# Kernel optimization log

Measured on AMD Instinct MI355X. Metric: run time of the kernel, lower is better.

## Reference

```python
import jax, jax.numpy as jnp
import numpy as np

N = 50000      # nodes
E = 800000     # edges
D_IN = 128
D_H = 128
D_OUT = 64
P = 0.3        # dropout prob


def _glorot(key, out_c, in_c):
    return jax.random.normal(key, (out_c, in_c), jnp.float32) * (1.0 / np.sqrt(in_c))


def setup_inputs() -> dict:
    key = jax.random.key(0)
    ks = jax.random.split(key, 10)
    return {
        "x": jax.random.normal(ks[0], (N, D_IN), jnp.float32),
        "u1": jax.random.uniform(ks[1], (N, D_H), jnp.float32),
        "u2": jax.random.uniform(ks[2], (N, D_H), jnp.float32),
        "wl0": _glorot(ks[3], D_H, D_IN), "bl0": jnp.zeros((D_H,), jnp.float32), "wr0": _glorot(ks[4], D_H, D_IN),
        "wl1": _glorot(ks[5], D_H, D_H), "bl1": jnp.zeros((D_H,), jnp.float32), "wr1": _glorot(ks[6], D_H, D_H),
        "wl2": _glorot(ks[7], D_OUT, D_H), "bl2": jnp.zeros((D_OUT,), jnp.float32), "wr2": _glorot(ks[8], D_OUT, D_H),
        "edge_index": jax.random.randint(ks[9], (2, E), 0, N),
    }


def _sage_conv(x, src, dst, wl, bl, wr):
    # PyG SAGEConv (aggr='mean'): lin_l(mean of neighbor msgs) + lin_r(x)
    msg = x[src]                                                    # [E, d] gather
    s = jax.ops.segment_sum(msg, dst, num_segments=N)               # [N, d] scatter-sum
    cnt = jax.ops.segment_sum(jnp.ones((dst.shape[0],), x.dtype), dst, num_segments=N)
    mean = s / jnp.maximum(cnt, 1.0)[:, None]                       # mean; 0 for isolated nodes
    return mean @ wl.T + bl + x @ wr.T


def reference(x, u1, u2, wl0, bl0, wr0, wl1, bl1, wr1, wl2, bl2, wr2, edge_index):
    src, dst = edge_index[0], edge_index[1]
    keep = 1.0 - P
    h = jax.nn.relu(_sage_conv(x, src, dst, wl0, bl0, wr0))
    h = h * ((u1 >= P).astype(h.dtype) / keep)                      # dropout (training=True)
    h = jax.nn.relu(_sage_conv(h, src, dst, wl1, bl1, wr1))
    h = h * ((u2 >= P).astype(h.dtype) / keep)
    return _sage_conv(h, src, dst, wl2, bl2, wr2)
```

## Files before the change

kernel.cpp:

```cpp
#include <hip/hip_runtime.h>


constexpr int N = 50000;
constexpr int E = 800000;
constexpr int NBUCK = (N + 255) / 256;
constexpr int CE = 4096;
constexpr int NEB = (E + CE - 1) / CE;
constexpr int SLOT = 5120;
static_assert(N <= 65536, "u16 packing");

typedef _Float16 f16x8 __attribute__((ext_vector_type(8)));
typedef _Float16 f16x2 __attribute__((ext_vector_type(2)));
typedef float f32x4 __attribute__((ext_vector_type(4)));


__global__ __launch_bounds__(256) void bucket_scatter_kernel(
    const int* __restrict__ src, const int* __restrict__ dst,
    int* __restrict__ bcur, unsigned* __restrict__ T) {
  __shared__ unsigned sorted[CE];
  __shared__ int hist[256], scan[256], excl[256], lcur[256], gbase[256];
  const int t = threadIdx.x;
  const int e0 = blockIdx.x * CE;
  const int nval = min(CE, E - e0);
  hist[t] = 0;
  __syncthreads();
  for (int i = t; i < nval; i += 256) atomicAdd(&hist[dst[e0 + i] >> 8], 1);
  __syncthreads();
  const int h = hist[t];
  scan[t] = h;
  __syncthreads();
  for (int off = 1; off < 256; off <<= 1) {
    int u = (t >= off) ? scan[t - off] : 0;
    __syncthreads();
    scan[t] += u;
    __syncthreads();
  }
  excl[t] = scan[t] - h;
  lcur[t] = scan[t] - h;
  gbase[t] = (t < NBUCK && h > 0) ? atomicAdd(&bcur[t], h) : 0;
  __syncthreads();
  for (int i = t; i < nval; i += 256) {
    int e = e0 + i;
    int d = dst[e];
    int p = atomicAdd(&lcur[d >> 8], 1);
    sorted[p] = ((unsigned)d << 16) | (unsigned)src[e];
  }
  __syncthreads();
  for (int i = t; i < nval; i += 256) {
    unsigned pk = sorted[i];
    int b = pk >> 24;
    T[gbase[b] + (i - excl[b])] = pk;
  }
}

__global__ __launch_bounds__(256) void bucket_place_kernel(
    const unsigned* __restrict__ T, const int* __restrict__ bcur,
    int* __restrict__ offs, int* __restrict__ deg, int* __restrict__ elist) {
  __shared__ int dcnt[256], s[256], ncur[256];
  const int t = threadIdx.x;
  const int b = blockIdx.x;
  const int lo = b * SLOT;
  const int hi = bcur[b];
  dcnt[t] = 0;
  __syncthreads();
  for (int i = lo + t; i < hi; i += 256) atomicAdd(&dcnt[(T[i] >> 16) & 255], 1);
  __syncthreads();
  const int v = dcnt[t];
  s[t] = v;
  __syncthreads();
  for (int off = 1; off < 256; off <<= 1) {
    int u = (t >= off) ? s[t - off] : 0;
    __syncthreads();
    s[t] += u;
    __syncthreads();
  }
  const int base = lo + s[t] - v;
  const int node = b * 256 + t;
  if (node < N) { offs[node] = base; deg[node] = v; }
  ncur[t] = base;
  __syncthreads();
  for (int i = lo + t; i < hi; i += 256) {
    unsigned pk = T[i];
    int pos = atomicAdd(&ncur[(pk >> 16) & 255], 1);
    elist[pos] = (int)(pk & 0xffffu);
  }
}

__device__ inline void wfrag_build(int idx, int KB, const float* wl,
                                   const float* wr, _Float16* wf) {
  int j = idx & 7;
  int lane = (idx >> 3) & 63;
  int kb = (idx >> 9) % KB;
  int ct = (idx >> 9) / KB;
  int c = ct * 16 + (lane & 15);
  int k = kb * 32 + (lane >> 4) * 8 + j;
  float v = (k < 128) ? wl[c * 128 + k] : wr[c * 128 + (k - 128)];
  wf[idx] = (_Float16)v;
}

constexpr int CONVB = (N * 128 / 8 + 255) / 256;

__global__ __launch_bounds__(256) void setup_kernel(
    const float* __restrict__ x,
    const float* __restrict__ wl0, const float* __restrict__ wr0,
    const float* __restrict__ wl1, const float* __restrict__ wr1,
    const float* __restrict__ wl2, const float* __restrict__ wr2,
    _Float16* __restrict__ HA, _Float16* __restrict__ wf0,
    _Float16* __restrict__ wf1, _Float16* __restrict__ wfZ,
    int* __restrict__ bcur) {
  const int b = blockIdx.x;
  const int t = threadIdx.x;
  if (b < CONVB) {
    int i = b * 256 + t;
    if (i < N * 128 / 8) {
      float4 a = ((const float4*)x)[i * 2];
      float4 c = ((const float4*)x)[i * 2 + 1];
      f16x8 v;
      v[0] = (_Float16)a.x; v[1] = (_Float16)a.y; v[2] = (_Float16)a.z; v[3] = (_Float16)a.w;
      v[4] = (_Float16)c.x; v[5] = (_Float16)c.y; v[6] = (_Float16)c.z; v[7] = (_Float16)c.w;
      ((f16x8*)HA)[i] = v;
    }
  } else if (b < CONVB + 128) {
    wfrag_build((b - CONVB) * 256 + t, 8, wl0, wr0, wf0);
  } else if (b < CONVB + 256) {
    wfrag_build((b - CONVB - 128) * 256 + t, 8, wl1, wr1, wf1);
  } else if (b < CONVB + 320) {
    int idx = (b - CONVB - 256) * 256 + t;
    int j = idx & 7;
    int lane = (idx >> 3) & 63;
    int kb = (idx >> 9) & 3;
    int ct = idx >> 11;
    int c = ct * 16 + (lane & 15);
    int k = kb * 32 + (lane >> 4) * 8 + j;
    float v = (c < 64) ? wl2[c * 128 + k] : wr2[(c - 64) * 128 + k];
    wfZ[idx] = (_Float16)v;
  } else {
    if (t < NBUCK) bcur[t] = t * SLOT;
  }
}

__global__ __launch_bounds__(256) void gather128_kernel(
    const _Float16* __restrict__ H, const int* __restrict__ offs,
    const int* __restrict__ deg, const int* __restrict__ elist,
    _Float16* __restrict__ M) {
  int node = blockIdx.x * 4 + (threadIdx.x >> 6);
  if (node >= N) return;
  int l = threadIdx.x & 63;
  const int e0 = offs[node];
  const int d = deg[node];
  const int e1 = e0 + d;
  float a0 = 0.f, a1 = 0.f;
  int e = e0;
  for (; e + 16 <= e1; e += 16) {
    int s[16];
#pragma unroll
    for (int u = 0; u < 16; ++u) s[u] = elist[e + u];
    f16x2 v[16];
#pragma unroll
    for (int u = 0; u < 16; ++u)
      v[u] = *(const f16x2*)(H + (size_t)s[u] * 128 + l * 2);
#pragma unroll
    for (int u = 0; u < 16; ++u) { a0 += (float)v[u][0]; a1 += (float)v[u][1]; }
  }
  for (; e + 4 <= e1; e += 4) {
    int s[4];
#pragma unroll
    for (int u = 0; u < 4; ++u) s[u] = elist[e + u];
    f16x2 v[4];
#pragma unroll
    for (int u = 0; u < 4; ++u)
      v[u] = *(const f16x2*)(H + (size_t)s[u] * 128 + l * 2);
#pragma unroll
    for (int u = 0; u < 4; ++u) { a0 += (float)v[u][0]; a1 += (float)v[u][1]; }
  }
  for (; e < e1; ++e) {
    f16x2 v = *(const f16x2*)(H + (size_t)elist[e] * 128 + l * 2);
    a0 += (float)v[0]; a1 += (float)v[1];
  }
  float inv = 1.0f / (float)max(d, 1);
  f16x2 o;
  o[0] = (_Float16)(a0 * inv); o[1] = (_Float16)(a1 * inv);
  *(f16x2*)(M + (size_t)node * 128 + l * 2) = o;
}

__global__ __launch_bounds__(256) void gather64_add_kernel(
    const _Float16* __restrict__ Y2, const float* __restrict__ F,
    const int* __restrict__ offs, const int* __restrict__ deg,
    const int* __restrict__ elist, float* __restrict__ out) {
  int node = blockIdx.x * 8 + (threadIdx.x >> 5);
  if (node >= N) return;
  int l = threadIdx.x & 31;
  const int e0 = offs[node];
  const int d = deg[node];
  const int e1 = e0 + d;
  float a0 = 0.f, a1 = 0.f;
  int e = e0;
  for (; e + 16 <= e1; e += 16) {
    int s[16];
#pragma unroll
    for (int u = 0; u < 16; ++u) s[u] = elist[e + u];
    f16x2 v[16];
#pragma unroll
    for (int u = 0; u < 16; ++u)
      v[u] = *(const f16x2*)(Y2 + (size_t)s[u] * 64 + l * 2);
#pragma unroll
    for (int u = 0; u < 16; ++u) { a0 += (float)v[u][0]; a1 += (float)v[u][1]; }
  }
  for (; e + 4 <= e1; e += 4) {
    int s[4];
#pragma unroll
    for (int u = 0; u < 4; ++u) s[u] = elist[e + u];
    f16x2 v[4];
#pragma unroll
    for (int u = 0; u < 4; ++u)
      v[u] = *(const f16x2*)(Y2 + (size_t)s[u] * 64 + l * 2);
#pragma unroll
    for (int u = 0; u < 4; ++u) { a0 += (float)v[u][0]; a1 += (float)v[u][1]; }
  }
  for (; e < e1; ++e) {
    f16x2 v = *(const f16x2*)(Y2 + (size_t)elist[e] * 64 + l * 2);
    a0 += (float)v[0]; a1 += (float)v[1];
  }
  float inv = 1.0f / (float)max(d, 1);
  float2 f = ((const float2*)(F + (size_t)node * 64))[l];
  float2 o;
  o.x = f.x + a0 * inv;
  o.y = f.y + a1 * inv;
  ((float2*)(out + (size_t)node * 64))[l] = o;
}

__global__ __launch_bounds__(256, 4) void mfma_gemm128_kernel(
    const _Float16* __restrict__ Mm, const _Float16* __restrict__ Hh,
    const _Float16* __restrict__ Wf, const float* __restrict__ bias,
    const float* __restrict__ U, _Float16* __restrict__ outp) {
  const int lane = threadIdx.x & 63;
  const int w = threadIdx.x >> 6;
  const int n16 = lane & 15;
  const int q = lane >> 4;
  const int rowbase = blockIdx.x * 32;
  const int colbase = w * 32;

  f32x4 acc[2][2];
#pragma unroll
  for (int h = 0; h < 2; ++h)
#pragma unroll
    for (int ct = 0; ct < 2; ++ct) acc[h][ct] = (f32x4){0.f, 0.f, 0.f, 0.f};

  int ar0 = min(rowbase + n16, N - 1);
  int ar1 = min(rowbase + 16 + n16, N - 1);
  const _Float16* pM0 = Mm + (size_t)ar0 * 128 + q * 8;
  const _Float16* pM1 = Mm + (size_t)ar1 * 128 + q * 8;
  const _Float16* pH0 = Hh + (size_t)ar0 * 128 + q * 8;
  const _Float16* pH1 = Hh + (size_t)ar1 * 128 + q * 8;

#pragma unroll
  for (int kb = 0; kb < 8; ++kb) {
    const int ko = (kb & 3) * 32;
    f16x8 a0 = *(const f16x8*)((kb < 4 ? pM0 : pH0) + ko);
    f16x8 a1 = *(const f16x8*)((kb < 4 ? pM1 : pH1) + ko);
#pragma unroll
    for (int ct = 0; ct < 2; ++ct) {
      const int ctg = w * 2 + ct;
      f16x8 b = *(const f16x8*)(Wf + ((size_t)(ctg * 8 + kb) * 64 + lane) * 8);
      acc[0][ct] = __builtin_amdgcn_mfma_f32_16x16x32_f16(a0, b, acc[0][ct], 0, 0, 0);
      acc[1][ct] = __builtin_amdgcn_mfma_f32_16x16x32_f16(a1, b, acc[1][ct], 0, 0, 0);
    }
  }

#pragma unroll
  for (int h = 0; h < 2; ++h) {
#pragma unroll
    for (int ct = 0; ct < 2; ++ct) {
      const int col = colbase + ct * 16 + n16;
      const float bv = bias[col];
#pragma unroll
      for (int r = 0; r < 4; ++r) {
        int row = rowbase + h * 16 + q * 4 + r;
        if (row < N) {
          float v = fmaxf(acc[h][ct][r] + bv, 0.f);
          float u = U[(size_t)row * 128 + col];
          v *= (u >= 0.3f) ? (1.0f / 0.7f) : 0.0f;
          outp[(size_t)row * 128 + col] = (_Float16)v;
        }
      }
    }
  }
}

__global__ __launch_bounds__(256, 4) void mfma_gemmZ_kernel(
    const _Float16* __restrict__ Hh, const _Float16* __restrict__ Wf,
    const float* __restrict__ bl2, _Float16* __restrict__ Y2,
    float* __restrict__ F) {
  const int lane = threadIdx.x & 63;
  const int w = threadIdx.x >> 6;
  const int n16 = lane & 15;
  const int q = lane >> 4;
  const int rowbase = blockIdx.x * 32;
  const int colbase = w * 32;

  f32x4 acc[2][2];
#pragma unroll
  for (int h = 0; h < 2; ++h)
#pragma unroll
    for (int ct = 0; ct < 2; ++ct) acc[h][ct] = (f32x4){0.f, 0.f, 0.f, 0.f};

  int ar0 = min(rowbase + n16, N - 1);
  int ar1 = min(rowbase + 16 + n16, N - 1);
  const _Float16* pH0 = Hh + (size_t)ar0 * 128 + q * 8;
  const _Float16* pH1 = Hh + (size_t)ar1 * 128 + q * 8;

#pragma unroll
  for (int kb = 0; kb < 4; ++kb) {
    const int ko = kb * 32;
    f16x8 a0 = *(const f16x8*)(pH0 + ko);
    f16x8 a1 = *(const f16x8*)(pH1 + ko);
#pragma unroll
    for (int ct = 0; ct < 2; ++ct) {
      const int ctg = w * 2 + ct;
      f16x8 b = *(const f16x8*)(Wf + ((size_t)(ctg * 4 + kb) * 64 + lane) * 8);
      acc[0][ct] = __builtin_amdgcn_mfma_f32_16x16x32_f16(a0, b, acc[0][ct], 0, 0, 0);
      acc[1][ct] = __builtin_amdgcn_mfma_f32_16x16x32_f16(a1, b, acc[1][ct], 0, 0, 0);
    }
  }

#pragma unroll
  for (int h = 0; h < 2; ++h) {
#pragma unroll
    for (int ct = 0; ct < 2; ++ct) {
      const int col = colbase + ct * 16 + n16;
#pragma unroll
      for (int r = 0; r < 4; ++r) {
        int row = rowbase + h * 16 + q * 4 + r;
        if (row < N) {
          float v = acc[h][ct][r];
          if (col < 64) Y2[(size_t)row * 64 + col] = (_Float16)v;
          else F[(size_t)row * 64 + (col - 64)] = v + bl2[col - 64];
        }
      }
    }
  }
}

extern "C" void kernel_launch(void* const* d_in, const int* in_sizes, int n_in,
                              void* d_out, int out_size, void* d_ws, size_t ws_size,
                              hipStream_t stream) {
  const float* x   = (const float*)d_in[0];
  const float* u1  = (const float*)d_in[1];
  const float* u2  = (const float*)d_in[2];
  const float* wl0 = (const float*)d_in[3];
  const float* bl0 = (const float*)d_in[4];
  const float* wr0 = (const float*)d_in[5];
  const float* wl1 = (const float*)d_in[6];
  const float* bl1 = (const float*)d_in[7];
  const float* wr1 = (const float*)d_in[8];
  const float* wl2 = (const float*)d_in[9];
  const float* bl2 = (const float*)d_in[10];
  const float* wr2 = (const float*)d_in[11];
  const int* edge  = (const int*)d_in[12];
  const int* src = edge;
  const int* dst = edge + E;

  _Float16* HA  = (_Float16*)d_ws;
  _Float16* HB  = HA + (size_t)N * 128;
  _Float16* M16 = HB + (size_t)N * 128;
  float* F      = (float*)(M16 + (size_t)N * 128);
  int* offs     = (int*)(F + (size_t)N * 64);
  int* deg      = offs + N;
  int* elist    = deg + N;
  unsigned* T   = (unsigned*)(elist + NBUCK * SLOT);
  int* bcur     = (int*)(T + NBUCK * SLOT);
  uintptr_t p = (uintptr_t)(bcur + NBUCK);
  p = (p + 15) & ~(uintptr_t)15;
  _Float16* wf0 = (_Float16*)p;
  _Float16* wf1 = wf0 + 8 * 8 * 512;
  _Float16* wfZ = wf1 + 8 * 8 * 512;

  setup_kernel<<<CONVB + 321, 256, 0, stream>>>(
      x, wl0, wr0, wl1, wr1, wl2, wr2, HA, wf0, wf1, wfZ, bcur);
  bucket_scatter_kernel<<<NEB, 256, 0, stream>>>(src, dst, bcur, T);
  bucket_place_kernel<<<NBUCK, 256, 0, stream>>>(T, bcur, offs, deg, elist);

  const int GG128 = (N + 3) / 4;
  const int GG64  = (N + 7) / 8;
  const int GM    = (N + 31) / 32;

  gather128_kernel<<<GG128, 256, 0, stream>>>(HA, offs, deg, elist, M16);
  mfma_gemm128_kernel<<<GM, 256, 0, stream>>>(M16, HA, wf0, bl0, u1, HB);
  gather128_kernel<<<GG128, 256, 0, stream>>>(HB, offs, deg, elist, M16);
  mfma_gemm128_kernel<<<GM, 256, 0, stream>>>(M16, HB, wf1, bl1, u2, HA);
  mfma_gemmZ_kernel<<<GM, 256, 0, stream>>>(HA, wfZ, bl2, M16, F);
  gather64_add_kernel<<<GG64, 256, 0, stream>>>(M16, F, offs, deg, elist,
                                                (float*)d_out);
}
```

Before: 308.7 us.

## Fuse neighbor-mean gather with MFMA GEMM per layer via shared memory

```diff
diff --git a/kernel.cpp b/kernel.cpp
--- a/kernel.cpp
+++ b/kernel.cpp
@@ -4,12 +4,13 @@
 constexpr int N = 50000;
 constexpr int E = 800000;
 constexpr int NBUCK = (N + 255) / 256;
-constexpr int CE = 4096;
+constexpr int CE = 2048;
 constexpr int NEB = (E + CE - 1) / CE;
 constexpr int SLOT = 5120;
 static_assert(N <= 65536, "u16 packing");
 
 typedef _Float16 f16x8 __attribute__((ext_vector_type(8)));
+typedef _Float16 f16x4 __attribute__((ext_vector_type(4)));
 typedef _Float16 f16x2 __attribute__((ext_vector_type(2)));
 typedef float f32x4 __attribute__((ext_vector_type(4)));
 
@@ -139,48 +140,111 @@
   }
 }
 
-__global__ __launch_bounds__(256) void gather128_kernel(
+__global__ __launch_bounds__(256, 4) void fused_layer_kernel(
     const _Float16* __restrict__ H, const int* __restrict__ offs,
     const int* __restrict__ deg, const int* __restrict__ elist,
-    _Float16* __restrict__ M) {
-  int node = blockIdx.x * 4 + (threadIdx.x >> 6);
-  if (node >= N) return;
-  int l = threadIdx.x & 63;
-  const int e0 = offs[node];
-  const int d = deg[node];
-  const int e1 = e0 + d;
-  float a0 = 0.f, a1 = 0.f;
-  int e = e0;
-  for (; e + 16 <= e1; e += 16) {
-    int s[16];
-#pragma unroll
-    for (int u = 0; u < 16; ++u) s[u] = elist[e + u];
-    f16x2 v[16];
-#pragma unroll
-    for (int u = 0; u < 16; ++u)
-      v[u] = *(const f16x2*)(H + (size_t)s[u] * 128 + l * 2);
-#pragma unroll
-    for (int u = 0; u < 16; ++u) { a0 += (float)v[u][0]; a1 += (float)v[u][1]; }
-  }
-  for (; e + 4 <= e1; e += 4) {
-    int s[4];
-#pragma unroll
-    for (int u = 0; u < 4; ++u) s[u] = elist[e + u];
-    f16x2 v[4];
-#pragma unroll
-    for (int u = 0; u < 4; ++u)
-      v[u] = *(const f16x2*)(H + (size_t)s[u] * 128 + l * 2);
-#pragma unroll
-    for (int u = 0; u < 4; ++u) { a0 += (float)v[u][0]; a1 += (float)v[u][1]; }
-  }
-  for (; e < e1; ++e) {
-    f16x2 v = *(const f16x2*)(H + (size_t)elist[e] * 128 + l * 2);
-    a0 += (float)v[0]; a1 += (float)v[1];
-  }
-  float inv = 1.0f / (float)max(d, 1);
-  f16x2 o;
-  o[0] = (_Float16)(a0 * inv); o[1] = (_Float16)(a1 * inv);
-  *(f16x2*)(M + (size_t)node * 128 + l * 2) = o;
+    const _Float16* __restrict__ Wf, const float* __restrict__ bias,
+    const float* __restrict__ U, _Float16* __restrict__ outp) {
+  __shared__ __align__(16) _Float16 Af[2][8][64][8];
+  const int t = threadIdx.x;
+  const int rowbase = blockIdx.x * 32;
+
+#pragma unroll
+  for (int m2 = 0; m2 < 2; ++m2) {
+    int m = t * 2 + m2;
+    int r = m >> 4, o = m & 15;
+    int row = min(rowbase + r, N - 1);
+    f16x8 v = *(const f16x8*)(H + (size_t)row * 128 + o * 8);
+    *(f16x8*)&Af[r >> 4][4 + (o >> 2)][(o & 3) * 16 + (r & 15)][0] = v;
+  }
+
+  {
+    const int hw = t >> 5;
+    const int ll = t & 31;
+    const int kb = ll >> 3, q = (ll >> 1) & 3, j = (ll & 1) * 4;
+#pragma unroll 1
+    for (int i = 0; i < 4; ++i) {
+      int r = hw * 4 + i;
+      int node = rowbase + r;
+      float a0 = 0.f, a1 = 0.f, a2 = 0.f, a3 = 0.f;
+      int d = 0;
+      if (node < N) {
+        const int e0 = offs[node];
+        d = deg[node];
+        const int e1 = e0 + d;
+        int e = e0;
+        for (; e + 8 <= e1; e += 8) {
+          int s[8];
+#pragma unroll
+          for (int u = 0; u < 8; ++u) s[u] = elist[e + u];
+          f16x4 v[8];
+#pragma unroll
+          for (int u = 0; u < 8; ++u)
+            v[u] = *(const f16x4*)(H + (size_t)s[u] * 128 + ll * 4);
+#pragma unroll
+          for (int u = 0; u < 8; ++u) {
+            a0 += (float)v[u][0]; a1 += (float)v[u][1];
+            a2 += (float)v[u][2]; a3 += (float)v[u][3];
+          }
+        }
+        for (; e < e1; ++e) {
+          f16x4 v = *(const f16x4*)(H + (size_t)elist[e] * 128 + ll * 4);
+          a0 += (float)v[0]; a1 += (float)v[1];
+          a2 += (float)v[2]; a3 += (float)v[3];
+        }
+      }
+      float inv = 1.0f / (float)max(d, 1);
+      f16x4 o;
+      o[0] = (_Float16)(a0 * inv); o[1] = (_Float16)(a1 * inv);
+      o[2] = (_Float16)(a2 * inv); o[3] = (_Float16)(a3 * inv);
+      *(f16x4*)&Af[r >> 4][kb][q * 16 + (r & 15)][j] = o;
+    }
+  }
+  __syncthreads();
+
+  const int lane = t & 63;
+  const int w = t >> 6;
+  const int n16 = lane & 15;
+  const int qq = lane >> 4;
+  const int colbase = w * 32;
+
+  f32x4 acc[2][2];
+#pragma unroll
+  for (int h = 0; h < 2; ++h)
+#pragma unroll
+    for (int ct = 0; ct < 2; ++ct) acc[h][ct] = (f32x4){0.f, 0.f, 0.f, 0.f};
+
+#pragma unroll
+  for (int kb = 0; kb < 8; ++kb) {
+    f16x8 a0 = *(const f16x8*)&Af[0][kb][lane][0];
+    f16x8 a1 = *(const f16x8*)&Af[1][kb][lane][0];
+#pragma unroll
+    for (int ct = 0; ct < 2; ++ct) {
+      const int ctg = w * 2 + ct;
+      f16x8 b = *(const f16x8*)(Wf + ((size_t)(ctg * 8 + kb) * 64 + lane) * 8);
+      acc[0][ct] = __builtin_amdgcn_mfma_f32_16x16x32_f16(a0, b, acc[0][ct], 0, 0, 0);
+      acc[1][ct] = __builtin_amdgcn_mfma_f32_16x16x32_f16(a1, b, acc[1][ct], 0, 0, 0);
+    }
+  }
+
+#pragma unroll
+  for (int h = 0; h < 2; ++h) {
+#pragma unroll
+    for (int ct = 0; ct < 2; ++ct) {
+      const int col = colbase + ct * 16 + n16;
+      const float bv = bias[col];
+#pragma unroll
+      for (int r = 0; r < 4; ++r) {
+        int row = rowbase + h * 16 + qq * 4 + r;
+        if (row < N) {
+          float v = fmaxf(acc[h][ct][r] + bv, 0.f);
+          float u = U[(size_t)row * 128 + col];
+          v *= (u >= 0.3f) ? (1.0f / 0.7f) : 0.0f;
+          outp[(size_t)row * 128 + col] = (_Float16)v;
+        }
+      }
+    }
+  }
 }
 
 __global__ __launch_bounds__(256) void gather64_add_kernel(
@@ -227,64 +291,6 @@
   o.x = f.x + a0 * inv;
   o.y = f.y + a1 * inv;
   ((float2*)(out + (size_t)node * 64))[l] = o;
-}
-
-__global__ __launch_bounds__(256, 4) void mfma_gemm128_kernel(
-    const _Float16* __restrict__ Mm, const _Float16* __restrict__ Hh,
-    const _Float16* __restrict__ Wf, const float* __restrict__ bias,
-    const float* __restrict__ U, _Float16* __restrict__ outp) {
-  const int lane = threadIdx.x & 63;
-  const int w = threadIdx.x >> 6;
-  const int n16 = lane & 15;
-  const int q = lane >> 4;
-  const int rowbase = blockIdx.x * 32;
-  const int colbase = w * 32;
-
-  f32x4 acc[2][2];
-#pragma unroll
-  for (int h = 0; h < 2; ++h)
-#pragma unroll
-    for (int ct = 0; ct < 2; ++ct) acc[h][ct] = (f32x4){0.f, 0.f, 0.f, 0.f};
-
-  int ar0 = min(rowbase + n16, N - 1);
-  int ar1 = min(rowbase + 16 + n16, N - 1);
-  const _Float16* pM0 = Mm + (size_t)ar0 * 128 + q * 8;
-  const _Float16* pM1 = Mm + (size_t)ar1 * 128 + q * 8;
-  const _Float16* pH0 = Hh + (size_t)ar0 * 128 + q * 8;
-  const _Float16* pH1 = Hh + (size_t)ar1 * 128 + q * 8;
-
-#pragma unroll
-  for (int kb = 0; kb < 8; ++kb) {
-    const int ko = (kb & 3) * 32;
-    f16x8 a0 = *(const f16x8*)((kb < 4 ? pM0 : pH0) + ko);
-    f16x8 a1 = *(const f16x8*)((kb < 4 ? pM1 : pH1) + ko);
-#pragma unroll
-    for (int ct = 0; ct < 2; ++ct) {
-      const int ctg = w * 2 + ct;
-      f16x8 b = *(const f16x8*)(Wf + ((size_t)(ctg * 8 + kb) * 64 + lane) * 8);
-      acc[0][ct] = __builtin_amdgcn_mfma_f32_16x16x32_f16(a0, b, acc[0][ct], 0, 0, 0);
-      acc[1][ct] = __builtin_amdgcn_mfma_f32_16x16x32_f16(a1, b, acc[1][ct], 0, 0, 0);
-    }
-  }
-
-#pragma unroll
-  for (int h = 0; h < 2; ++h) {
-#pragma unroll
-    for (int ct = 0; ct < 2; ++ct) {
-      const int col = colbase + ct * 16 + n16;
-      const float bv = bias[col];
-#pragma unroll
-      for (int r = 0; r < 4; ++r) {
-        int row = rowbase + h * 16 + q * 4 + r;
-        if (row < N) {
-          float v = fmaxf(acc[h][ct][r] + bv, 0.f);
-          float u = U[(size_t)row * 128 + col];
-          v *= (u >= 0.3f) ? (1.0f / 0.7f) : 0.0f;
-          outp[(size_t)row * 128 + col] = (_Float16)v;
-        }
-      }
-    }
-  }
 }
 
 __global__ __launch_bounds__(256, 4) void mfma_gemmZ_kernel(
@@ -380,14 +386,11 @@
   bucket_scatter_kernel<<<NEB, 256, 0, stream>>>(src, dst, bcur, T);
   bucket_place_kernel<<<NBUCK, 256, 0, stream>>>(T, bcur, offs, deg, elist);
 
-  const int GG128 = (N + 3) / 4;
-  const int GG64  = (N + 7) / 8;
-  const int GM    = (N + 31) / 32;
-
-  gather128_kernel<<<GG128, 256, 0, stream>>>(HA, offs, deg, elist, M16);
-  mfma_gemm128_kernel<<<GM, 256, 0, stream>>>(M16, HA, wf0, bl0, u1, HB);
-  gather128_kernel<<<GG128, 256, 0, stream>>>(HB, offs, deg, elist, M16);
-  mfma_gemm128_kernel<<<GM, 256, 0, stream>>>(M16, HB, wf1, bl1, u2, HA);
+  const int GM   = (N + 31) / 32;
+  const int GG64 = (N + 7) / 8;
+
+  fused_layer_kernel<<<GM, 256, 0, stream>>>(HA, offs, deg, elist, wf0, bl0, u1, HB);
+  fused_layer_kernel<<<GM, 256, 0, stream>>>(HB, offs, deg, elist, wf1, bl1, u2, HA);
   mfma_gemmZ_kernel<<<GM, 256, 0, stream>>>(HA, wfZ, bl2, M16, F);
   gather64_add_kernel<<<GG64, 256, 0, stream>>>(M16, F, offs, deg, elist,
                                                 (float*)d_out);
```

After: 290.3 us. 1.06x faster.
